# Kernel optimization log

Measured on AMD Instinct MI355X. Metric: run time of the kernel, lower is better.

## Reference

```python
import jax, jax.numpy as jnp
import numpy as np

D = 1024  # d_model (all ATTENTION_CONST widths)
N = 4096  # sequence length


def setup_inputs() -> dict:
    key = jax.random.key(0)
    ks = jax.random.split(key, 11)
    s = 1.0 / np.sqrt(D)
    return {
        "q": jax.random.normal(ks[0], (N, D), jnp.float32),
        "k": jax.random.normal(ks[1], (N, D), jnp.float32),
        "v": jax.random.normal(ks[2], (N, D), jnp.float32),
        "wq_w": jax.random.normal(ks[3], (D, D), jnp.float32) * s,
        "wq_b": jax.random.normal(ks[4], (D,), jnp.float32) * s,
        "wk_w": jax.random.normal(ks[5], (D, D), jnp.float32) * s,
        "wk_b": jax.random.normal(ks[6], (D,), jnp.float32) * s,
        "wv_w": jax.random.normal(ks[7], (D, D), jnp.float32) * s,
        "wv_b": jax.random.normal(ks[8], (D,), jnp.float32) * s,
        "wo_w": jax.random.normal(ks[9], (D, D), jnp.float32) * s,
        "wo_b": jax.random.normal(ks[10], (D,), jnp.float32) * s,
    }


def reference(q, k, v, wq_w, wq_b, wk_w, wk_b, wv_w, wv_b, wo_w, wo_b):
    # Linear projections (torch convention: y = x @ W.T + b)
    qp = q @ wq_w.T + wq_b  # [N, D]
    kp = k @ wk_w.T + wk_b  # [N, D]
    vp = v @ wv_w.T + wv_b  # [N, D]
    # Naive attention: NO sqrt(d) scaling, NO head split (faithful to source)
    scores = qp @ kp.T                      # [N, N]
    attention_weights = jax.nn.softmax(scores, axis=-1)
    x = attention_weights @ vp              # [N, D]
    x = x @ wo_w.T + wo_b                   # output projection
    return (x, attention_weights)
```

## Files before the change

kernel.cpp:

```cpp
#include <hip/hip_runtime.h>
#include <cstdint>

#define N_SEQ 4096
#define DMODEL 1024

#define BM 128
#define BN 128
#define BN2 64
#define UNITE 4096

typedef __bf16 bf16_t;
typedef _Float16 f16_t;
typedef f16_t f16x8 __attribute__((ext_vector_type(8)));
typedef f16_t f16x4 __attribute__((ext_vector_type(4)));
typedef float f32x4 __attribute__((ext_vector_type(4)));

typedef __attribute__((address_space(1))) void* as1ptr;
typedef __attribute__((address_space(3))) void* as3ptr;

__device__ __forceinline__ void gload16(const void* g, void* l) {
  __builtin_amdgcn_global_load_lds((as1ptr)(uintptr_t)g, (as3ptr)(uintptr_t)l,
                                   16, 0, 0);
}

#define SBAR() asm volatile("s_barrier" ::: "memory")
#define WAITLGKM(n)                                              \
  do {                                                           \
    asm volatile("s_waitcnt lgkmcnt(" #n ")" ::: "memory");      \
    __builtin_amdgcn_sched_barrier(0);                           \
  } while (0)
#define WAITVM(n) asm volatile("s_waitcnt vmcnt(" #n ")" ::: "memory")

__global__ __launch_bounds__(256)
void qkv_proj(const f16_t* __restrict__ qh, const f16_t* __restrict__ ql,
              const f16_t* __restrict__ wq, const float* __restrict__ wq_b,
              const f16_t* __restrict__ kh, const f16_t* __restrict__ kl,
              const f16_t* __restrict__ wk, const float* __restrict__ wk_b,
              const f16_t* __restrict__ vh, const f16_t* __restrict__ wv,
              const float* __restrict__ wv_b,
              f16_t* __restrict__ QPh, f16_t* __restrict__ QPl,
              f16_t* __restrict__ KPh, f16_t* __restrict__ VPt)
{
  __shared__ __align__(16) f16_t lds[6 * UNITE];

  const int z = blockIdx.z;
  const f16_t *A0, *A1 = nullptr, *B0;
  const float* bias;
  if (z == 0)      { A0 = qh; A1 = ql; B0 = wq; bias = wq_b; }
  else if (z == 1) { A0 = kh; A1 = kl; B0 = wk; bias = wk_b; }
  else             { A0 = vh;          B0 = wv; bias = wv_b; }
  const bool twop = (z < 2);

  const int M = N_SEQ, Nc = DMODEL, K = DMODEL;
  const int t = threadIdx.x;
  const int lane = t & 63;
  const int wave = t >> 6;
  const int wm = wave >> 1;
  const int wn = wave & 1;

  const int gx = gridDim.x;
  const int nwg = gx * gridDim.y;
  const int flat = blockIdx.y * gx + blockIdx.x;
  const int swz = (flat & 7) * (nwg >> 3) + (flat >> 3);
  const int row0 = (swz / gx) * BM;
  const int col0 = (swz % gx) * BN;

  const int srw = t >> 3;
  const int scol = 8 * ((t & 7) ^ ((t >> 3) & 7));
  const int sdst = t * 8;

  const int fr = lane & 15;
  const int kq = (lane >> 4) * 8;
  const int sw = (fr & 7) << 3;

  f32x4 acc[4][4] = {};

  for (int k0 = 0; k0 < K; k0 += 64) {
#pragma unroll
    for (int h = 0; h < 2; ++h) {
      const int r = h * 32 + srw;
      gload16(A0 + (size_t)(row0 + r) * K + k0 + scol,
              &lds[0 * UNITE + h * 2048 + sdst]);
      gload16(A0 + (size_t)(row0 + 64 + r) * K + k0 + scol,
              &lds[1 * UNITE + h * 2048 + sdst]);
      gload16(B0 + (size_t)(col0 + r) * K + k0 + scol,
              &lds[4 * UNITE + h * 2048 + sdst]);
      gload16(B0 + (size_t)(col0 + 64 + r) * K + k0 + scol,
              &lds[5 * UNITE + h * 2048 + sdst]);
      if (twop) {
        gload16(A1 + (size_t)(row0 + r) * K + k0 + scol,
                &lds[2 * UNITE + h * 2048 + sdst]);
        gload16(A1 + (size_t)(row0 + 64 + r) * K + k0 + scol,
                &lds[3 * UNITE + h * 2048 + sdst]);
      }
    }
    __syncthreads();

    f16x8 ah[4][2], al[4][2], bh[4][2];
#pragma unroll
    for (int m = 0; m < 4; ++m) {
      const int r = (m * 16 + fr) * 64;
#pragma unroll
      for (int ks = 0; ks < 2; ++ks) {
        const int c = (ks * 32 + kq) ^ sw;
        ah[m][ks] = *(const f16x8*)&lds[wm * UNITE + r + c];
        if (twop) al[m][ks] = *(const f16x8*)&lds[(2 + wm) * UNITE + r + c];
      }
    }
#pragma unroll
    for (int n = 0; n < 4; ++n) {
      const int r = (n * 16 + fr) * 64;
#pragma unroll
      for (int ks = 0; ks < 2; ++ks)
        bh[n][ks] = *(const f16x8*)&lds[(4 + wn) * UNITE + r +
                                        (((ks * 32 + kq)) ^ sw)];
    }

#pragma unroll
    for (int m = 0; m < 4; ++m)
#pragma unroll
      for (int n = 0; n < 4; ++n)
#pragma unroll
        for (int ks = 0; ks < 2; ++ks) {
          acc[m][n] = __builtin_amdgcn_mfma_f32_16x16x32_f16(
              ah[m][ks], bh[n][ks], acc[m][n], 0, 0, 0);
          if (twop)
            acc[m][n] = __builtin_amdgcn_mfma_f32_16x16x32_f16(
                al[m][ks], bh[n][ks], acc[m][n], 0, 0, 0);
        }
    __syncthreads();
  }

#pragma unroll
  for (int m = 0; m < 4; ++m) {
#pragma unroll
    for (int n = 0; n < 4; ++n) {
      const int grow0 = row0 + wm * 64 + m * 16 + (lane >> 4) * 4;
      const int gcol = col0 + wn * 64 + n * 16 + (lane & 15);
      const float bv = bias[gcol];
      if (z == 2) {
        f16x4 p;
#pragma unroll
        for (int r = 0; r < 4; ++r) p[r] = (f16_t)(acc[m][n][r] + bv);
        *(f16x4*)&VPt[(size_t)gcol * M + grow0] = p;
      } else if (z == 0) {
#pragma unroll
        for (int r = 0; r < 4; ++r) {
          const float val = acc[m][n][r] + bv;
          const size_t idx = (size_t)(grow0 + r) * Nc + gcol;
          const f16_t h = (f16_t)val;
          QPh[idx] = h;
          QPl[idx] = (f16_t)(val - (float)h);
        }
      } else {
#pragma unroll
        for (int r = 0; r < 4; ++r) {
          const float val = acc[m][n][r] + bv;
          KPh[(size_t)(grow0 + r) * Nc + gcol] = (f16_t)val;
        }
      }
    }
  }
}

template <int OUT_F32>
__global__ __launch_bounds__(256)
void gemm_f16p(const f16_t* __restrict__ A, const f16_t* __restrict__ B,
               const float* __restrict__ bias,
               f16_t* __restrict__ Cf16, float* __restrict__ Cf32,
               int M, int Nc, int K)
{
  __shared__ __align__(16) f16_t lds[2 * 3 * UNITE];

  const int gx = gridDim.x;
  const int nwg = gx * gridDim.y;
  const int flat = blockIdx.y * gx + blockIdx.x;
  const int swz = (flat & 7) * (nwg >> 3) + (flat >> 3);
  const int bx = swz % gx;
  const int by = swz / gx;

  const int t = threadIdx.x;
  const int lane = t & 63;
  const int wave = t >> 6;
  const int wm = wave >> 1;
  const int wn = wave & 1;
  const int row0 = by * BM;
  const int col0 = bx * BN2;

  const int srw = t >> 3;
  const int scol = 8 * ((t & 7) ^ ((t >> 3) & 7));
  const int sdst = t * 8;

  const int fr = lane & 15;
  const int kq = (lane >> 4) * 8;
  const int sw = (fr & 7) << 3;

  auto stage = [&](int buf, int kt) {
    const int k0 = kt << 6;
#pragma unroll
    for (int h = 0; h < 2; ++h) {
      const int r = h * 32 + srw;
      gload16(A + (size_t)(row0 + r) * K + k0 + scol,
              &lds[(buf * 3 + 0) * UNITE + h * 2048 + sdst]);
      gload16(A + (size_t)(row0 + 64 + r) * K + k0 + scol,
              &lds[(buf * 3 + 1) * UNITE + h * 2048 + sdst]);
      gload16(B + (size_t)(col0 + r) * K + k0 + scol,
              &lds[(buf * 3 + 2) * UNITE + h * 2048 + sdst]);
    }
  };

  f32x4 acc[4][2] = {};
  const int NT = K >> 6;

  stage(0, 0);
  stage(1, 1);
  WAITVM(6);
  SBAR();

  for (int kt = 0; kt < NT; ++kt) {
    const int p = kt & 1;
    const f16_t* Ab = &lds[(p * 3 + wm) * UNITE];
    const f16_t* Bb = &lds[(p * 3 + 2) * UNITE];

    f16x8 ah[4][2], bh[2][2];
#pragma unroll
    for (int m = 0; m < 2; ++m)
#pragma unroll
      for (int ks = 0; ks < 2; ++ks)
        ah[m][ks] = *(const f16x8*)&Ab[(m * 16 + fr) * 64 +
                                       ((ks * 32 + kq) ^ sw)];
#pragma unroll
    for (int n = 0; n < 2; ++n)
#pragma unroll
      for (int ks = 0; ks < 2; ++ks)
        bh[n][ks] = *(const f16x8*)&Bb[(wn * 32 + n * 16 + fr) * 64 +
                                       ((ks * 32 + kq) ^ sw)];
#pragma unroll
    for (int m = 2; m < 4; ++m)
#pragma unroll
      for (int ks = 0; ks < 2; ++ks)
        ah[m][ks] = *(const f16x8*)&Ab[(m * 16 + fr) * 64 +
                                       ((ks * 32 + kq) ^ sw)];

    WAITLGKM(4);
#pragma unroll
    for (int m = 0; m < 2; ++m)
#pragma unroll
      for (int n = 0; n < 2; ++n)
#pragma unroll
        for (int ks = 0; ks < 2; ++ks)
          acc[m][n] = __builtin_amdgcn_mfma_f32_16x16x32_f16(
              ah[m][ks], bh[n][ks], acc[m][n], 0, 0, 0);
    WAITLGKM(0);
#pragma unroll
    for (int m = 2; m < 4; ++m)
#pragma unroll
      for (int n = 0; n < 2; ++n)
#pragma unroll
        for (int ks = 0; ks < 2; ++ks)
          acc[m][n] = __builtin_amdgcn_mfma_f32_16x16x32_f16(
              ah[m][ks], bh[n][ks], acc[m][n], 0, 0, 0);

    SBAR();
    if (kt + 2 < NT) {
      stage(p, kt + 2);
      WAITVM(6);
    } else if (kt + 1 < NT) {
      WAITVM(0);
    }
    SBAR();
  }

#pragma unroll
  for (int m = 0; m < 4; ++m) {
#pragma unroll
    for (int n = 0; n < 2; ++n) {
      const int grow0 = row0 + wm * 64 + m * 16 + (lane >> 4) * 4;
      const int gcol = col0 + wn * 32 + n * 16 + (lane & 15);
#pragma unroll
      for (int r = 0; r < 4; ++r) {
        const size_t idx = (size_t)(grow0 + r) * Nc + gcol;
        if (OUT_F32) Cf32[idx] = acc[m][n][r] + bias[gcol];
        else         Cf16[idx] = (f16_t)acc[m][n][r];
      }
    }
  }
}

#define TILE_ELEMS 16384
#define UNIT_ELEMS 4096
#define NT_SC 32

template <int V> struct ic { static constexpr int value = V; };

template <int MH>
__device__ __forceinline__ void load_A8f(const f16_t* Ab, int wm, int fr,
                                         int kq, int sw, f16x8 (&af)[4][2]) {
#pragma unroll
  for (int m = 0; m < 4; ++m) {
    const int row = wm * 128 + (MH * 4 + m) * 16 + fr;
#pragma unroll
    for (int ks = 0; ks < 2; ++ks)
      af[m][ks] = *(const f16x8*)&Ab[row * 64 + ((ks * 32 + kq) ^ sw)];
  }
}

template <int NH>
__device__ __forceinline__ void load_B4f(const f16_t* Bb, int wn, int fr,
                                         int kq, int sw, f16x8 (&bfr)[2][2]) {
#pragma unroll
  for (int n = 0; n < 2; ++n) {
    const int row = wn * 64 + (NH * 2 + n) * 16 + fr;
#pragma unroll
    for (int ks = 0; ks < 2; ++ks)
      bfr[n][ks] = *(const f16x8*)&Bb[row * 64 + ((ks * 32 + kq) ^ sw)];
  }
}

template <int MH, int NH>
__device__ __forceinline__ void mfma16f(const f16x8 (&af)[4][2],
                                        const f16x8 (&bfr)[2][2],
                                        f32x4 (&acc)[8][4]) {
#pragma unroll
  for (int m = 0; m < 4; ++m)
#pragma unroll
    for (int n = 0; n < 2; ++n)
#pragma unroll
      for (int ks = 0; ks < 2; ++ks)
        acc[MH * 4 + m][NH * 2 + n] = __builtin_amdgcn_mfma_f32_16x16x32_f16(
            af[m][ks], bfr[n][ks], acc[MH * 4 + m][NH * 2 + n], 0, 0, 0);
}

__global__ __launch_bounds__(512, 1)
void gemm8f_scores(const f16_t* __restrict__ Qh, const f16_t* __restrict__ Ql,
                   const f16_t* __restrict__ Kh, float* __restrict__ C)
{
  __shared__ __align__(16) f16_t sm[2 * 2 * TILE_ELEMS];

  const int t = threadIdx.x;
  const int lane = t & 63;
  const int wave = t >> 6;
  const int wm = wave >> 2;
  const int wn = wave & 3;

  const int flat = blockIdx.y * 16 + blockIdx.x;
  const int swzb = (flat & 7) * 32 + (flat >> 3);
  const int brow = (swzb >> 4) * 256;
  const int bcol = (swzb & 15) * 256;

  const int srow = t >> 3;
  const int scol = 8 * ((t & 7) ^ ((t >> 3) & 7));
  const int sdst = t * 8;

  const int fr = lane & 15;
  const int kq = (lane >> 4) * 8;
  const int sw = (fr & 7) << 3;

  auto stageA = [&](int buf, int u, int kt) {
    const f16_t* src = (kt >= 16) ? Ql : Qh;
    const int kk = (kt & 15) << 6;
    gload16(src + (size_t)(brow + u * 64 + srow) * DMODEL + kk + scol,
            &sm[(buf * 2 + 0) * TILE_ELEMS + u * UNIT_ELEMS + sdst]);
  };
  auto stageB = [&](int buf, int u, int kt) {
    const int kk = (kt & 15) << 6;
    gload16(Kh + (size_t)(bcol + u * 64 + srow) * DMODEL + kk + scol,
            &sm[(buf * 2 + 1) * TILE_ELEMS + u * UNIT_ELEMS + sdst]);
  };

  f32x4 acc[8][4] = {};
  f16x8 af0[4][2], af1[4][2];
  f16x8 b0[2][2], b1[2][2];

#pragma unroll
  for (int u = 0; u < 4; ++u) stageA(0, u, 0);
#pragma unroll
  for (int u = 0; u < 4; ++u) stageB(0, u, 0);
  stageA(1, 0, 1); stageA(1, 2, 1);
  stageB(1, 0, 1); stageB(1, 1, 1);
  stageA(1, 1, 1); stageA(1, 3, 1);
  WAITVM(6);
  SBAR();

  auto tile = [&](auto Pc, int kt) {
    constexpr int p = decltype(Pc)::value;
    constexpr int q = p ^ 1;
    const bool n1 = (kt + 1 < NT_SC);
    const bool n2 = (kt + 2 < NT_SC);
    const f16_t* Ab = &sm[(p * 2 + 0) * TILE_ELEMS];
    const f16_t* Bb = &sm[(p * 2 + 1) * TILE_ELEMS];

    load_A8f<0>(Ab, wm, fr, kq, sw, af0);
    load_B4f<0>(Bb, wn, fr, kq, sw, b0);
    if (n1) { stageB(q, 2, kt + 1); stageB(q, 3, kt + 1); }
    load_B4f<1>(Bb, wn, fr, kq, sw, b1);
    WAITLGKM(4);
    __builtin_amdgcn_s_setprio(1);
    mfma16f<0, 0>(af0, b0, acc);
    __builtin_amdgcn_s_setprio(0);
    __builtin_amdgcn_sched_barrier(0);
    SBAR();

    if (n2) { stageA(p, 0, kt + 2); stageA(p, 2, kt + 2); }
    load_A8f<1>(Ab, wm, fr, kq, sw, af1);
    WAITLGKM(8);
    __builtin_amdgcn_s_setprio(1);
    mfma16f<0, 1>(af0, b1, acc);
    __builtin_amdgcn_s_setprio(0);
    __builtin_amdgcn_sched_barrier(0);
    SBAR();

    if (n2) { stageB(p, 0, kt + 2); stageB(p, 1, kt + 2); }
    WAITLGKM(0);
    __builtin_amdgcn_s_setprio(1);
    mfma16f<1, 0>(af1, b0, acc);
    __builtin_amdgcn_s_setprio(0);
    __builtin_amdgcn_sched_barrier(0);
    SBAR();

    if (n2) { stageA(p, 1, kt + 2); stageA(p, 3, kt + 2); }
    __builtin_amdgcn_s_setprio(1);
    mfma16f<1, 1>(af1, b1, acc);
    __builtin_amdgcn_s_setprio(0);
    __builtin_amdgcn_sched_barrier(0);
    if (n2)      WAITVM(6);
    else if (n1) WAITVM(0);
    SBAR();
  };

  for (int kt = 0; kt < NT_SC; kt += 2) {
    tile(ic<0>{}, kt);
    tile(ic<1>{}, kt + 1);
  }

#pragma unroll
  for (int mf = 0; mf < 8; ++mf) {
#pragma unroll
    for (int nf = 0; nf < 4; ++nf) {
      const int r0 = brow + wm * 128 + mf * 16 + (lane >> 4) * 4;
      const int c  = bcol + wn * 64 + nf * 16 + (lane & 15);
#pragma unroll
      for (int r = 0; r < 4; ++r)
        C[(size_t)(r0 + r) * N_SEQ + c] = acc[mf][nf][r];
    }
  }
}

struct SplitDesc {
  const float* src[7];
  f16_t* hi[7];
  f16_t* lo[7];
  int mode[7];
  int blk_start[8];
};

__global__ __launch_bounds__(256)
void split_all(SplitDesc d)
{
  const int b = blockIdx.x;
  int seg = 0;
#pragma unroll
  for (int s = 1; s < 7; ++s) seg += (b >= d.blk_start[s]) ? 1 : 0;
  const int i = (b - d.blk_start[seg]) * 256 + threadIdx.x;
  const float4 v = ((const float4*)d.src[seg])[i];
  const float vv[4] = {v.x, v.y, v.z, v.w};
  f16x4 h, l;
#pragma unroll
  for (int j = 0; j < 4; ++j) {
    const f16_t hh = (f16_t)vv[j];
    h[j] = hh;
    l[j] = (f16_t)(vv[j] - (float)hh);
  }
  ((f16x4*)d.hi[seg])[i] = h;
  if (d.mode[seg] == 2) ((f16x4*)d.lo[seg])[i] = l;
}

__global__ __launch_bounds__(256)
void softmax_rows(float* __restrict__ S, f16_t* __restrict__ P, int n)
{
  const int row = blockIdx.x;
  float* srow = S + (size_t)row * n;
  f16_t* prow = P + (size_t)row * n;
  const int t = threadIdx.x;
  const int lane = t & 63;
  const int wave = t >> 6;
  __shared__ float red[8];

  float4 v[4];
  float mx = -3.4e38f;
#pragma unroll
  for (int i = 0; i < 4; ++i) {
    v[i] = *(const float4*)(srow + (size_t)(i * 256 + t) * 4);
    mx = fmaxf(mx, fmaxf(fmaxf(v[i].x, v[i].y), fmaxf(v[i].z, v[i].w)));
  }
#pragma unroll
  for (int off = 32; off > 0; off >>= 1) mx = fmaxf(mx, __shfl_xor(mx, off));
  if (lane == 0) red[wave] = mx;
  __syncthreads();
  mx = fmaxf(fmaxf(red[0], red[1]), fmaxf(red[2], red[3]));

  float e[16];
  float sum = 0.f;
#pragma unroll
  for (int i = 0; i < 4; ++i) {
    e[4 * i + 0] = __expf(v[i].x - mx);
    e[4 * i + 1] = __expf(v[i].y - mx);
    e[4 * i + 2] = __expf(v[i].z - mx);
    e[4 * i + 3] = __expf(v[i].w - mx);
    sum += e[4 * i + 0] + e[4 * i + 1] + e[4 * i + 2] + e[4 * i + 3];
  }
#pragma unroll
  for (int off = 32; off > 0; off >>= 1) sum += __shfl_xor(sum, off);
  if (lane == 0) red[4 + wave] = sum;
  __syncthreads();
  sum = red[4] + red[5] + red[6] + red[7];
  const float inv = 1.0f / sum;

#pragma unroll
  for (int i = 0; i < 4; ++i) {
    float4 w;
    w.x = e[4 * i + 0] * inv;
    w.y = e[4 * i + 1] * inv;
    w.z = e[4 * i + 2] * inv;
    w.w = e[4 * i + 3] * inv;
    *(float4*)(srow + (size_t)(i * 256 + t) * 4) = w;
    f16x4 p;
    p[0] = (f16_t)w.x;
    p[1] = (f16_t)w.y;
    p[2] = (f16_t)w.z;
    p[3] = (f16_t)w.w;
    *(f16x4*)(prow + (size_t)(i * 256 + t) * 4) = p;
  }
}

extern "C" void kernel_launch(void* const* d_in, const int* in_sizes, int n_in,
                              void* d_out, int out_size, void* d_ws, size_t ws_size,
                              hipStream_t stream) {
  const int N = N_SEQ, D = DMODEL;
  const float* q    = (const float*)d_in[0];
  const float* k    = (const float*)d_in[1];
  const float* v    = (const float*)d_in[2];
  const float* wq_w = (const float*)d_in[3];
  const float* wq_b = (const float*)d_in[4];
  const float* wk_w = (const float*)d_in[5];
  const float* wk_b = (const float*)d_in[6];
  const float* wv_w = (const float*)d_in[7];
  const float* wv_b = (const float*)d_in[8];
  const float* wo_w = (const float*)d_in[9];
  const float* wo_b = (const float*)d_in[10];

  float* x_out = (float*)d_out;
  float* attn  = x_out + (size_t)N * D;

  char* wsp = (char*)d_ws;
  auto alloc = [&](size_t bytes) { char* p = wsp; wsp += bytes; return p; };
  const size_t ND = (size_t)N * D, DD = (size_t)D * D;
  f16_t*  qh16  = (f16_t*)alloc(ND * 2);
  f16_t*  ql16  = (f16_t*)alloc(ND * 2);
  f16_t*  kh16  = (f16_t*)alloc(ND * 2);
  f16_t*  kl16  = (f16_t*)alloc(ND * 2);
  f16_t*  vh16  = (f16_t*)alloc(ND * 2);
  f16_t*  wq16  = (f16_t*)alloc(DD * 2);
  f16_t*  wk16  = (f16_t*)alloc(DD * 2);
  f16_t*  wv16  = (f16_t*)alloc(DD * 2);
  f16_t*  wo16  = (f16_t*)alloc(DD * 2);
  f16_t*  QPh   = (f16_t*)alloc(ND * 2);
  f16_t*  QPl   = (f16_t*)alloc(ND * 2);
  f16_t*  KPh   = (f16_t*)alloc(ND * 2);
  f16_t*  spare = (f16_t*)alloc(ND * 2);
  f16_t*  VPt   = (f16_t*)alloc(ND * 2);
  f16_t*  Pb    = QPh;
  f16_t*  Xb    = vh16;
  (void)spare;

  SplitDesc sd;
  sd.src[0] = q;    sd.hi[0] = qh16;  sd.lo[0] = ql16;    sd.mode[0] = 2;
  sd.src[1] = k;    sd.hi[1] = kh16;  sd.lo[1] = kl16;    sd.mode[1] = 2;
  sd.src[2] = v;    sd.hi[2] = vh16;  sd.lo[2] = nullptr; sd.mode[2] = 3;
  sd.src[3] = wq_w; sd.hi[3] = wq16;  sd.lo[3] = nullptr; sd.mode[3] = 3;
  sd.src[4] = wk_w; sd.hi[4] = wk16;  sd.lo[4] = nullptr; sd.mode[4] = 3;
  sd.src[5] = wv_w; sd.hi[5] = wv16;  sd.lo[5] = nullptr; sd.mode[5] = 3;
  sd.src[6] = wo_w; sd.hi[6] = wo16;  sd.lo[6] = nullptr; sd.mode[6] = 3;
  const int nb_nd = (int)(ND / 4 / 256);
  const int nb_dd = (int)(DD / 4 / 256);
  sd.blk_start[0] = 0;
  sd.blk_start[1] = nb_nd;
  sd.blk_start[2] = 2 * nb_nd;
  sd.blk_start[3] = 3 * nb_nd;
  sd.blk_start[4] = 3 * nb_nd + nb_dd;
  sd.blk_start[5] = 3 * nb_nd + 2 * nb_dd;
  sd.blk_start[6] = 3 * nb_nd + 3 * nb_dd;
  sd.blk_start[7] = 3 * nb_nd + 4 * nb_dd;
  split_all<<<dim3(sd.blk_start[7]), dim3(256), 0, stream>>>(sd);

  const dim3 blk(256);
  const dim3 gsc(N / 256, N / 256);
  const dim3 gd(D / BN2, N / BM);

  qkv_proj<<<dim3(D / BN, N / BM, 3), blk, 0, stream>>>(
      qh16, ql16, wq16, wq_b,
      kh16, kl16, wk16, wk_b,
      vh16, wv16, wv_b,
      QPh, QPl, KPh, VPt);

  gemm8f_scores<<<gsc, dim3(512), 0, stream>>>(QPh, QPl, KPh, attn);

  softmax_rows<<<dim3(N), blk, 0, stream>>>(attn, Pb, N);

  gemm_f16p<0><<<gd, blk, 0, stream>>>(
      Pb, VPt, nullptr, Xb, nullptr, N, D, N);

  gemm_f16p<1><<<gd, blk, 0, stream>>>(
      Xb, wo16, wo_b, nullptr, x_out, N, D, D);
}
```

Baseline: 219.4 us.

## Move precision split from scores GEMM into K projection weights

The scores GEMM no longer runs a second K-pass over a low-order QP residual, which halves its K loop (NT_SC 32 to 16). To keep accuracy, the K projection now also splits wk_w into hi/lo f16 halves and does a third MFMA per step, and the Q projection writes only a single f16 output. This trades a larger, more costly scores GEMM (4096x4096x2048) for a small extra pass in the 4096x1024x1024 projection. It risks lower accuracy on the scores, since QP is now rounded to a single f16.

```diff
diff --git a/kernel.cpp b/kernel.cpp
--- a/kernel.cpp
+++ b/kernel.cpp
@@ -35,21 +35,23 @@
 void qkv_proj(const f16_t* __restrict__ qh, const f16_t* __restrict__ ql,
               const f16_t* __restrict__ wq, const float* __restrict__ wq_b,
               const f16_t* __restrict__ kh, const f16_t* __restrict__ kl,
-              const f16_t* __restrict__ wk, const float* __restrict__ wk_b,
+              const f16_t* __restrict__ wkh, const f16_t* __restrict__ wkl,
+              const float* __restrict__ wk_b,
               const f16_t* __restrict__ vh, const f16_t* __restrict__ wv,
               const float* __restrict__ wv_b,
-              f16_t* __restrict__ QPh, f16_t* __restrict__ QPl,
-              f16_t* __restrict__ KPh, f16_t* __restrict__ VPt)
+              f16_t* __restrict__ QPh, f16_t* __restrict__ KPh,
+              f16_t* __restrict__ VPt)
 {
-  __shared__ __align__(16) f16_t lds[6 * UNITE];
+  __shared__ __align__(16) f16_t lds[8 * UNITE];
 
   const int z = blockIdx.z;
-  const f16_t *A0, *A1 = nullptr, *B0;
+  const f16_t *A0, *A1 = nullptr, *B0, *B1 = nullptr;
   const float* bias;
-  if (z == 0)      { A0 = qh; A1 = ql; B0 = wq; bias = wq_b; }
-  else if (z == 1) { A0 = kh; A1 = kl; B0 = wk; bias = wk_b; }
-  else             { A0 = vh;          B0 = wv; bias = wv_b; }
-  const bool twop = (z < 2);
+  if (z == 0)      { A0 = qh; A1 = ql; B0 = wq;               bias = wq_b; }
+  else if (z == 1) { A0 = kh; A1 = kl; B0 = wkh; B1 = wkl;    bias = wk_b; }
+  else             { A0 = vh;          B0 = wv;               bias = wv_b; }
+  const bool p2 = (z < 2);
+  const bool p3 = (z == 1);
 
   const int M = N_SEQ, Nc = DMODEL, K = DMODEL;
   const int t = threadIdx.x;
@@ -87,16 +89,22 @@
               &lds[4 * UNITE + h * 2048 + sdst]);
       gload16(B0 + (size_t)(col0 + 64 + r) * K + k0 + scol,
               &lds[5 * UNITE + h * 2048 + sdst]);
-      if (twop) {
+      if (p2) {
         gload16(A1 + (size_t)(row0 + r) * K + k0 + scol,
                 &lds[2 * UNITE + h * 2048 + sdst]);
         gload16(A1 + (size_t)(row0 + 64 + r) * K + k0 + scol,
                 &lds[3 * UNITE + h * 2048 + sdst]);
       }
+      if (p3) {
+        gload16(B1 + (size_t)(col0 + r) * K + k0 + scol,
+                &lds[6 * UNITE + h * 2048 + sdst]);
+        gload16(B1 + (size_t)(col0 + 64 + r) * K + k0 + scol,
+                &lds[7 * UNITE + h * 2048 + sdst]);
+      }
     }
     __syncthreads();
 
-    f16x8 ah[4][2], al[4][2], bh[4][2];
+    f16x8 ah[4][2], al[4][2], bh[4][2], bl[4][2];
 #pragma unroll
     for (int m = 0; m < 4; ++m) {
       const int r = (m * 16 + fr) * 64;
@@ -104,16 +112,18 @@
       for (int ks = 0; ks < 2; ++ks) {
         const int c = (ks * 32 + kq) ^ sw;
         ah[m][ks] = *(const f16x8*)&lds[wm * UNITE + r + c];
-        if (twop) al[m][ks] = *(const f16x8*)&lds[(2 + wm) * UNITE + r + c];
+        if (p2) al[m][ks] = *(const f16x8*)&lds[(2 + wm) * UNITE + r + c];
       }
     }
 #pragma unroll
     for (int n = 0; n < 4; ++n) {
       const int r = (n * 16 + fr) * 64;
 #pragma unroll
-      for (int ks = 0; ks < 2; ++ks)
-        bh[n][ks] = *(const f16x8*)&lds[(4 + wn) * UNITE + r +
-                                        (((ks * 32 + kq)) ^ sw)];
+      for (int ks = 0; ks < 2; ++ks) {
+        const int c = (ks * 32 + kq) ^ sw;
+        bh[n][ks] = *(const f16x8*)&lds[(4 + wn) * UNITE + r + c];
+        if (p3) bl[n][ks] = *(const f16x8*)&lds[(6 + wn) * UNITE + r + c];
+      }
     }
 
 #pragma unroll
@@ -124,9 +134,12 @@
         for (int ks = 0; ks < 2; ++ks) {
           acc[m][n] = __builtin_amdgcn_mfma_f32_16x16x32_f16(
               ah[m][ks], bh[n][ks], acc[m][n], 0, 0, 0);
-          if (twop)
+          if (p2)
             acc[m][n] = __builtin_amdgcn_mfma_f32_16x16x32_f16(
                 al[m][ks], bh[n][ks], acc[m][n], 0, 0, 0);
+          if (p3)
+            acc[m][n] = __builtin_amdgcn_mfma_f32_16x16x32_f16(
+                ah[m][ks], bl[n][ks], acc[m][n], 0, 0, 0);
         }
     __syncthreads();
   }
@@ -143,21 +156,11 @@
 #pragma unroll
         for (int r = 0; r < 4; ++r) p[r] = (f16_t)(acc[m][n][r] + bv);
         *(f16x4*)&VPt[(size_t)gcol * M + grow0] = p;
-      } else if (z == 0) {
-#pragma unroll
-        for (int r = 0; r < 4; ++r) {
-          const float val = acc[m][n][r] + bv;
-          const size_t idx = (size_t)(grow0 + r) * Nc + gcol;
-          const f16_t h = (f16_t)val;
-          QPh[idx] = h;
-          QPl[idx] = (f16_t)(val - (float)h);
-        }
       } else {
-#pragma unroll
-        for (int r = 0; r < 4; ++r) {
-          const float val = acc[m][n][r] + bv;
-          KPh[(size_t)(grow0 + r) * Nc + gcol] = (f16_t)val;
-        }
+        f16_t* out = (z == 0) ? QPh : KPh;
+#pragma unroll
+        for (int r = 0; r < 4; ++r)
+          out[(size_t)(grow0 + r) * Nc + gcol] = (f16_t)(acc[m][n][r] + bv);
       }
     }
   }
@@ -289,7 +292,7 @@
 
 #define TILE_ELEMS 16384
 #define UNIT_ELEMS 4096
-#define NT_SC 32
+#define NT_SC 16
 
 template <int V> struct ic { static constexpr int value = V; };
 
@@ -332,8 +335,8 @@
 }
 
 __global__ __launch_bounds__(512, 1)
-void gemm8f_scores(const f16_t* __restrict__ Qh, const f16_t* __restrict__ Ql,
-                   const f16_t* __restrict__ Kh, float* __restrict__ C)
+void gemm8f_scores(const f16_t* __restrict__ Qh, const f16_t* __restrict__ Kh,
+                   float* __restrict__ C)
 {
   __shared__ __align__(16) f16_t sm[2 * 2 * TILE_ELEMS];
 
@@ -357,13 +360,12 @@
   const int sw = (fr & 7) << 3;
 
   auto stageA = [&](int buf, int u, int kt) {
-    const f16_t* src = (kt >= 16) ? Ql : Qh;
-    const int kk = (kt & 15) << 6;
-    gload16(src + (size_t)(brow + u * 64 + srow) * DMODEL + kk + scol,
+    const int kk = kt << 6;
+    gload16(Qh + (size_t)(brow + u * 64 + srow) * DMODEL + kk + scol,
             &sm[(buf * 2 + 0) * TILE_ELEMS + u * UNIT_ELEMS + sdst]);
   };
   auto stageB = [&](int buf, int u, int kt) {
-    const int kk = (kt & 15) << 6;
+    const int kk = kt << 6;
     gload16(Kh + (size_t)(bcol + u * 64 + srow) * DMODEL + kk + scol,
             &sm[(buf * 2 + 1) * TILE_ELEMS + u * UNIT_ELEMS + sdst]);
   };
@@ -562,23 +564,24 @@
   f16_t*  vh16  = (f16_t*)alloc(ND * 2);
   f16_t*  wq16  = (f16_t*)alloc(DD * 2);
   f16_t*  wk16  = (f16_t*)alloc(DD * 2);
+  f16_t*  wk16l = (f16_t*)alloc(DD * 2);
   f16_t*  wv16  = (f16_t*)alloc(DD * 2);
   f16_t*  wo16  = (f16_t*)alloc(DD * 2);
   f16_t*  QPh   = (f16_t*)alloc(ND * 2);
-  f16_t*  QPl   = (f16_t*)alloc(ND * 2);
+  f16_t*  pad1  = (f16_t*)alloc(ND * 2);
   f16_t*  KPh   = (f16_t*)alloc(ND * 2);
-  f16_t*  spare = (f16_t*)alloc(ND * 2);
+  f16_t*  pad2  = (f16_t*)alloc(ND * 2);
   f16_t*  VPt   = (f16_t*)alloc(ND * 2);
   f16_t*  Pb    = QPh;
   f16_t*  Xb    = vh16;
-  (void)spare;
+  (void)pad1; (void)pad2;
 
   SplitDesc sd;
   sd.src[0] = q;    sd.hi[0] = qh16;  sd.lo[0] = ql16;    sd.mode[0] = 2;
   sd.src[1] = k;    sd.hi[1] = kh16;  sd.lo[1] = kl16;    sd.mode[1] = 2;
   sd.src[2] = v;    sd.hi[2] = vh16;  sd.lo[2] = nullptr; sd.mode[2] = 3;
   sd.src[3] = wq_w; sd.hi[3] = wq16;  sd.lo[3] = nullptr; sd.mode[3] = 3;
-  sd.src[4] = wk_w; sd.hi[4] = wk16;  sd.lo[4] = nullptr; sd.mode[4] = 3;
+  sd.src[4] = wk_w; sd.hi[4] = wk16;  sd.lo[4] = wk16l;   sd.mode[4] = 2;
   sd.src[5] = wv_w; sd.hi[5] = wv16;  sd.lo[5] = nullptr; sd.mode[5] = 3;
   sd.src[6] = wo_w; sd.hi[6] = wo16;  sd.lo[6] = nullptr; sd.mode[6] = 3;
   const int nb_nd = (int)(ND / 4 / 256);
@@ -599,11 +602,11 @@
 
   qkv_proj<<<dim3(D / BN, N / BM, 3), blk, 0, stream>>>(
       qh16, ql16, wq16, wq_b,
-      kh16, kl16, wk16, wk_b,
+      kh16, kl16, wk16, wk16l, wk_b,
       vh16, wv16, wv_b,
-      QPh, QPl, KPh, VPt);
-
-  gemm8f_scores<<<gsc, dim3(512), 0, stream>>>(QPh, QPl, KPh, attn);
+      QPh, KPh, VPt);
+
+  gemm8f_scores<<<gsc, dim3(512), 0, stream>>>(QPh, KPh, attn);
 
   softmax_rows<<<dim3(N), blk, 0, stream>>>(attn, Pb, N);
 
```

Result: no change. 218.6 us (-0.3%).
